# Performance work log

Hardware: AMD Instinct MI355X
Metric: run time of the kernel (lower is better)

## Reference

```python
import jax, jax.numpy as jnp
import numpy as np

H = 100  # hidden_size
D = 300  # input/output feature dim (hardcoded in module)
T = 32768  # number of timesteps


def _lstm_layer(x_seq, W_ih, W_hh, b_ih, b_hh):
    """Single LSTM layer over time. x_seq: [T, H_in]. PyTorch gate order i,f,g,o."""
    Hh = W_hh.shape[1]
    b = b_ih + b_hh
    # precompute input projection for all timesteps (removes per-step GEMM)
    x_proj = x_seq @ W_ih.T + b  # [T, 4H]

    def step(carry, xp_t):
        h, c = carry
        gates = xp_t + h @ W_hh.T  # [4H]
        i, f, g, o = jnp.split(gates, 4, axis=-1)
        c = jax.nn.sigmoid(f) * c + jax.nn.sigmoid(i) * jnp.tanh(g)
        h = jax.nn.sigmoid(o) * jnp.tanh(c)
        return (h, c), h

    h0 = jnp.zeros((Hh,), x_seq.dtype)
    c0 = jnp.zeros((Hh,), x_seq.dtype)
    (h_T, c_T), hs = jax.lax.scan(step, (h0, c0), x_proj)
    return hs, h_T, c_T


def setup_inputs() -> dict:
    key = jax.random.key(0)
    ks = jax.random.split(key, 14)
    s = 0.08
    return {
        "inputs": jax.random.normal(ks[0], (T, D), jnp.float32),
        "W_inp": jax.random.normal(ks[1], (H, D), jnp.float32) * s,
        "b_inp": jax.random.normal(ks[2], (H,), jnp.float32) * s,
        "W_ih_l0": jax.random.normal(ks[3], (4 * H, H), jnp.float32) * s,
        "W_hh_l0": jax.random.normal(ks[4], (4 * H, H), jnp.float32) * s,
        "b_ih_l0": jax.random.normal(ks[5], (4 * H,), jnp.float32) * s,
        "b_hh_l0": jax.random.normal(ks[6], (4 * H,), jnp.float32) * s,
        "W_ih_l1": jax.random.normal(ks[7], (4 * H, H), jnp.float32) * s,
        "W_hh_l1": jax.random.normal(ks[8], (4 * H, H), jnp.float32) * s,
        "b_ih_l1": jax.random.normal(ks[9], (4 * H,), jnp.float32) * s,
        "b_hh_l1": jax.random.normal(ks[10], (4 * H,), jnp.float32) * s,
        "W_out": jax.random.normal(ks[11], (D, H), jnp.float32) * s,
        "b_out": jax.random.normal(ks[12], (D,), jnp.float32) * s,
    }


def reference(inputs, W_inp, b_inp, W_ih_l0, W_hh_l0, b_ih_l0, b_hh_l0,
              W_ih_l1, W_hh_l1, b_ih_l1, b_hh_l1, W_out, b_out):
    # teacher-forced forward (force=True): input projection for all steps at once
    x = inputs @ W_inp.T + b_inp  # [T, H]
    h0_seq, h0_T, c0_T = _lstm_layer(x, W_ih_l0, W_hh_l0, b_ih_l0, b_hh_l0)
    h1_seq, h1_T, c1_T = _lstm_layer(h0_seq, W_ih_l1, W_hh_l1, b_ih_l1, b_hh_l1)
    outputs = h1_seq @ W_out.T + b_out  # [T, D]
    h_n = jnp.stack([h0_T, h1_T])  # [2, H] final hidden per layer
    c_n = jnp.stack([c0_T, c1_T])  # [2, H] final cell per layer
    return outputs, h_n, c_n
```

## Files before the change

### kernel.cpp

```cpp
#include <hip/hip_runtime.h>

#define T_STEPS 32768
#define OUT_BASE 9830400

typedef _Float16 h2 __attribute__((ext_vector_type(2)));

#define H2BC(f_) __builtin_bit_cast(h2, f_)

__device__ __forceinline__ float fdot2(h2 a, h2 b, float c) {
#if __has_builtin(__builtin_amdgcn_fdot2)
    return __builtin_amdgcn_fdot2(a, b, c, false);
#else
    return c + (float)a.x * (float)b.x + (float)a.y * (float)b.y;
#endif
}

__device__ __forceinline__ float sigf(float x) { return 1.f / (1.f + __expf(-x)); }

__device__ __forceinline__ float tanh_f(float x) {
    float a = fabsf(x);
    float e = __expf(-2.f * a);
    float t = (1.f - e) / (1.f + e);
    return x < 0.f ? -t : t;
}

template <int CTRL>
__device__ __forceinline__ float qperm(float x) {
#if __has_builtin(__builtin_amdgcn_update_dpp)
    return __builtin_bit_cast(
        float, __builtin_amdgcn_update_dpp(0, __builtin_bit_cast(int, x), CTRL, 0xF, 0xF, true));
#else
    return __shfl_xor(x, CTRL == 0xB1 ? 1 : (CTRL == 0x4E ? 2 : 3));
#endif
}

__device__ __forceinline__ void bar_lds() {
    asm volatile("s_waitcnt lgkmcnt(0)\n\ts_barrier" ::: "memory");
}

__global__ void k_precomp(const float* __restrict__ W_inp, const float* __restrict__ b_inp,
                          const float* __restrict__ W_ih0, const float* __restrict__ b_ih0,
                          const float* __restrict__ b_hh0,
                          float* __restrict__ Wc, float* __restrict__ bc) {
    int idx = blockIdx.x * 256 + threadIdx.x;
    if (idx < 120000) {
        int r = idx / 300, d = idx % 300;
        float acc = 0.f;
        for (int h = 0; h < 100; h++) acc += W_ih0[r * 100 + h] * W_inp[h * 300 + d];
        Wc[idx] = acc;
    } else if (idx < 120400) {
        int r = idx - 120000;
        float acc = b_ih0[r] + b_hh0[r];
        for (int h = 0; h < 100; h++) acc += W_ih0[r * 100 + h] * b_inp[h];
        bc[r] = acc;
    }
}

__global__ __launch_bounds__(512) void k_xproj(const float* __restrict__ inp,
                                               const float* __restrict__ Wc,
                                               const float* __restrict__ bc,
                                               _Float16* __restrict__ x0p) {
    __shared__ float xs[32 * 300];
    int t0 = blockIdx.x * 32;
    for (int idx = threadIdx.x; idx < 9600; idx += 512) xs[idx] = inp[(size_t)t0 * 300 + idx];
    __syncthreads();
    int j = threadIdx.x;
    if (j < 400) {
        float acc[32];
#pragma unroll
        for (int i = 0; i < 32; i++) acc[i] = 0.f;
        const float4* w4 = (const float4*)(Wc + j * 300);
        const float4* x4 = (const float4*)xs;
        for (int d4 = 0; d4 < 75; d4++) {
            float4 w = w4[d4];
#pragma unroll
            for (int ti = 0; ti < 32; ti++) {
                float4 x = x4[ti * 75 + d4];
                acc[ti] += w.x * x.x + w.y * x.y + w.z * x.z + w.w * x.w;
            }
        }
        float bb = bc[j];
        int dst = (j % 100) * 4 + j / 100;
#pragma unroll
        for (int ti = 0; ti < 32; ti++)
            x0p[(size_t)(t0 + ti) * 400 + dst] = (_Float16)(acc[ti] + bb);
    }
}


#define TICK0(T_, XREG_, TNEXT_, P_) do {                                                    \
    if (j < 400) {                                                                           \
        float xc_ = XREG_;                                                                   \
        int tn_ = (TNEXT_) < T_STEPS ? (TNEXT_) : T_STEPS - 1;                               \
        XREG_ = (float)x0p[(size_t)tn_ * 400 + j];                                           \
        const float4* h4_ = (const float4*)hbuf[P_];                                         \
        float aa_ = xc_, ab_ = 0.f, ac_ = 0.f, ad_ = 0.f;                                    \
        _Pragma("unroll")                                                                    \
        for (int c_ = 0; c_ < 12; c_++) {                                                    \
            float4 v_ = h4_[c_];                                                             \
            aa_ = fdot2(w0[4 * c_ + 0], H2BC(v_.x), aa_);                                    \
            ab_ = fdot2(w0[4 * c_ + 1], H2BC(v_.y), ab_);                                    \
            ac_ = fdot2(w0[4 * c_ + 2], H2BC(v_.z), ac_);                                    \
            ad_ = fdot2(w0[4 * c_ + 3], H2BC(v_.w), ad_);                                    \
        }                                                                                    \
        { float2 v_ = *(const float2*)((const char*)hbuf[P_] + 192);                         \
          aa_ = fdot2(w0[48], H2BC(v_.x), aa_);                                              \
          ab_ = fdot2(w0[49], H2BC(v_.y), ab_); }                                            \
        float s0_ = (aa_ + ab_) + (ac_ + ad_);                                               \
        float nl_ = __builtin_fmaf(sigf(s0_ * s_), s_, addc_);                               \
        float fg_ = qperm<0xB1>(nl_), gg_ = qperm<0x4E>(nl_), og_ = qperm<0x1B>(nl_);        \
        if ((j & 3) == 0) {                                                                  \
            int u_ = j >> 2;                                                                 \
            c0 = fg_ * c0 + nl_ * gg_;                                                       \
            float h0v_ = og_ * tanh_f(c0);                                                   \
            hbuf[1 - (P_)][u_] = (_Float16)h0v_;                                             \
            if ((T_) == T_STEPS - 1) { outTail[u_] = h0v_; outTail[200 + u_] = c0; }         \
        }                                                                                    \
    } else if (j >= 448) {                                                                   \
        int k_ = j - 448;                                                                    \
        if (k_ < 50 && (T_) >= 1) {                                                          \
            unsigned v_ = ((const unsigned*)hbuf[P_])[k_];                                   \
            __hip_atomic_store(&h0seq[(size_t)((T_) - 1) * 50 + k_], v_,                     \
                               __ATOMIC_RELAXED, __HIP_MEMORY_SCOPE_AGENT);                  \
        }                                                                                    \
        if (k_ == 0 && ((T_) & 7) == 7)                                                      \
            __hip_atomic_store(flag, (unsigned)(T_),                                         \
                               __ATOMIC_RELEASE, __HIP_MEMORY_SCOPE_AGENT);                  \
    }                                                                                        \
    bar_lds();                                                                               \
} while (0)

#define TICK1(T_, P_, WREG_, LREG_) do {                                                     \
    if (j < 400) {                                                                           \
        const char* hb_ = (const char*)hbuf[P_];                                             \
        const float4* u0_ = (const float4*)hb_;                                              \
        const float4* u1_ = (const float4*)(hb_ + 208);                                      \
        float aa_ = b1c, ab_ = 0.f, ac_ = 0.f, ad_ = 0.f;                                    \
        _Pragma("unroll")                                                                    \
        for (int c_ = 0; c_ < 12; c_++) {                                                    \
            float4 v_ = u0_[c_];                                                             \
            aa_ = fdot2(w1[4 * c_ + 0], H2BC(v_.x), aa_);                                    \
            ab_ = fdot2(w1[4 * c_ + 1], H2BC(v_.y), ab_);                                    \
            ac_ = fdot2(w1[4 * c_ + 2], H2BC(v_.z), ac_);                                    \
            ad_ = fdot2(w1[4 * c_ + 3], H2BC(v_.w), ad_);                                    \
        }                                                                                    \
        { float2 v_ = *(const float2*)(hb_ + 192);                                           \
          aa_ = fdot2(w1[48], H2BC(v_.x), aa_);                                              \
          ab_ = fdot2(w1[49], H2BC(v_.y), ab_); }                                            \
        _Pragma("unroll")                                                                    \
        for (int c_ = 0; c_ < 12; c_++) {                                                    \
            float4 v_ = u1_[c_];                                                             \
            aa_ = fdot2(w1[50 + 4 * c_ + 0], H2BC(v_.x), aa_);                               \
            ab_ = fdot2(w1[50 + 4 * c_ + 1], H2BC(v_.y), ab_);                               \
            ac_ = fdot2(w1[50 + 4 * c_ + 2], H2BC(v_.z), ac_);                               \
            ad_ = fdot2(w1[50 + 4 * c_ + 3], H2BC(v_.w), ad_);                               \
        }                                                                                    \
        { float2 v_ = *(const float2*)(hb_ + 400);                                           \
          aa_ = fdot2(w1[98], H2BC(v_.x), aa_);                                              \
          ab_ = fdot2(w1[99], H2BC(v_.y), ab_); }                                            \
        float s1_ = (aa_ + ab_) + (ac_ + ad_);                                               \
        float nl_ = __builtin_fmaf(sigf(s1_ * s_), s_, addc_);                               \
        float fg_ = qperm<0xB1>(nl_), gg_ = qperm<0x4E>(nl_), og_ = qperm<0x1B>(nl_);        \
        if ((j & 3) == 0) {                                                                  \
            int u_ = j >> 2;                                                                 \
            c1 = fg_ * c1 + nl_ * gg_;                                                       \
            float h1v_ = og_ * tanh_f(c1);                                                   \
            hbuf[1 - (P_)][104 + u_] = (_Float16)h1v_;                                       \
            h1s[(size_t)(T_) * 100 + u_] = h1v_;                                             \
            if ((T_) == T_STEPS - 1) { outTail[100 + u_] = h1v_; outTail[300 + u_] = c1; }   \
        }                                                                                    \
    } else if (j >= 448) {                                                                   \
        int k_ = j - 448;                                                                    \
        if (k_ < 50) {                                                                       \
            if ((T_) + 1 < T_STEPS) ((unsigned*)hbuf[1 - (P_)])[k_] = WREG_;                 \
            if ((T_) + 2 < T_STEPS) {                                                        \
                int need_ = (T_) + 3;                                                        \
                if ((int)fcache < need_) {                                                   \
                    unsigned f_;                                                             \
                    while ((int)(f_ = __hip_atomic_load(flag, __ATOMIC_RELAXED,              \
                                                        __HIP_MEMORY_SCOPE_AGENT)) < need_) \
                        __builtin_amdgcn_s_sleep(2);                                         \
                    fcache = f_;                                                             \
                    asm volatile("" ::: "memory");                                           \
                }                                                                            \
                LREG_ = __hip_atomic_load(&h0seq[(size_t)((T_) + 2) * 50 + k_],              \
                                          __ATOMIC_RELAXED, __HIP_MEMORY_SCOPE_AGENT);       \
            }                                                                                \
        }                                                                                    \
    }                                                                                        \
    bar_lds();                                                                               \
} while (0)

__global__ __launch_bounds__(512) __attribute__((amdgpu_waves_per_eu(2, 2)))
void k_scan2(const _Float16* __restrict__ x0p,
             const float* __restrict__ Whh0,
             const float* __restrict__ Wih1,
             const float* __restrict__ Whh1,
             const float* __restrict__ bih1,
             const float* __restrict__ bhh1,
             float* __restrict__ h1s,
             float* __restrict__ outTail,
             unsigned* __restrict__ h0seq,
             unsigned* __restrict__ flag) {
    __shared__ __align__(16) _Float16 hbuf[2][208];
    const int j = threadIdx.x;
    const int g4 = j & 3;
    const float s_ = (g4 == 2) ? 2.f : 1.f;
    const float addc_ = (g4 == 2) ? -1.f : 0.f;

    if (blockIdx.x == 0) {
        h2 w0[50];
        float xa = 0.f, xb = 0.f, c0 = 0.f;
        if (j < 400) {
            int r = g4 * 100 + (j >> 2);
            const float2* p0 = (const float2*)(Whh0 + r * 100);
#pragma unroll
            for (int k = 0; k < 50; k++) { float2 v = p0[k]; h2 q; q.x = (_Float16)v.x; q.y = (_Float16)v.y; w0[k] = q; }
            xa = (float)x0p[j];
            xb = (float)x0p[400 + j];
        }
        if (j < 208) ((unsigned*)hbuf)[j] = 0u;
        __syncthreads();

        for (int t = 0; t < T_STEPS; t += 2) {
            TICK0(t, xa, t + 2, 0);
            TICK0(t + 1, xb, t + 3, 1);
        }
        if (j >= 448) {
            int k = j - 448;
            if (k < 50) {
                unsigned v = ((const unsigned*)hbuf[0])[k];
                __hip_atomic_store(&h0seq[(size_t)(T_STEPS - 1) * 50 + k], v,
                                   __ATOMIC_RELAXED, __HIP_MEMORY_SCOPE_AGENT);
            }
            if (k == 0)
                __hip_atomic_store(flag, (unsigned)T_STEPS,
                                   __ATOMIC_RELEASE, __HIP_MEMORY_SCOPE_AGENT);
        }
    } else {
        h2 w1[100];
        float b1c = 0.f, c1 = 0.f;
        unsigned vA = 0, vB = 0, fcache = 0;
        if (j < 400) {
            int r = g4 * 100 + (j >> 2);
            const float2* p1 = (const float2*)(Wih1 + r * 100);
#pragma unroll
            for (int k = 0; k < 50; k++) { float2 v = p1[k]; h2 q; q.x = (_Float16)v.x; q.y = (_Float16)v.y; w1[k] = q; }
            const float2* p2 = (const float2*)(Whh1 + r * 100);
#pragma unroll
            for (int k = 0; k < 50; k++) { float2 v = p2[k]; h2 q; q.x = (_Float16)v.x; q.y = (_Float16)v.y; w1[50 + k] = q; }
            b1c = bih1[r] + bhh1[r];
        }
        if (j < 208) ((unsigned*)hbuf)[j] = 0u;
        __syncthreads();
        if (j >= 448) {
            int k = j - 448;
            unsigned f_;
            while ((int)(f_ = __hip_atomic_load(flag, __ATOMIC_RELAXED, __HIP_MEMORY_SCOPE_AGENT)) < 2)
                __builtin_amdgcn_s_sleep(8);
            fcache = f_;
            asm volatile("" ::: "memory");
            if (k < 50) {
                vA = __hip_atomic_load(&h0seq[k], __ATOMIC_RELAXED, __HIP_MEMORY_SCOPE_AGENT);
                vB = __hip_atomic_load(&h0seq[50 + k], __ATOMIC_RELAXED, __HIP_MEMORY_SCOPE_AGENT);
                ((unsigned*)hbuf[0])[k] = vA;
            }
        }
        __syncthreads();

        for (int t = 0; t < T_STEPS; t += 2) {
            TICK1(t, 0, vB, vA);
            TICK1(t + 1, 1, vA, vB);
        }
    }
}

__global__ __launch_bounds__(320) void k_out(const float* __restrict__ h1s,
                                             const float* __restrict__ Wout,
                                             const float* __restrict__ bout,
                                             float* __restrict__ out) {
    __shared__ float hs[32 * 100];
    int t0 = blockIdx.x * 32;
    for (int idx = threadIdx.x; idx < 3200; idx += 320) hs[idx] = h1s[(size_t)t0 * 100 + idx];
    __syncthreads();
    int d = threadIdx.x;
    if (d < 300) {
        float acc[32];
#pragma unroll
        for (int i = 0; i < 32; i++) acc[i] = 0.f;
        const float4* w4 = (const float4*)(Wout + d * 100);
        const float4* h4 = (const float4*)hs;
        for (int j4 = 0; j4 < 25; j4++) {
            float4 w = w4[j4];
#pragma unroll
            for (int ti = 0; ti < 32; ti++) {
                float4 h = h4[ti * 25 + j4];
                acc[ti] += w.x * h.x + w.y * h.y + w.z * h.z + w.w * h.w;
            }
        }
        float bb = bout[d];
#pragma unroll
        for (int ti = 0; ti < 32; ti++) out[(size_t)(t0 + ti) * 300 + d] = acc[ti] + bb;
    }
}

extern "C" void kernel_launch(void* const* d_in, const int* in_sizes, int n_in,
                              void* d_out, int out_size, void* d_ws, size_t ws_size,
                              hipStream_t stream) {
    const float* inputs = (const float*)d_in[0];
    const float* W_inp  = (const float*)d_in[1];
    const float* b_inp  = (const float*)d_in[2];
    const float* W_ih0  = (const float*)d_in[3];
    const float* W_hh0  = (const float*)d_in[4];
    const float* b_ih0  = (const float*)d_in[5];
    const float* b_hh0  = (const float*)d_in[6];
    const float* W_ih1  = (const float*)d_in[7];
    const float* W_hh1  = (const float*)d_in[8];
    const float* b_ih1  = (const float*)d_in[9];
    const float* b_hh1  = (const float*)d_in[10];
    const float* W_out  = (const float*)d_in[11];
    const float* b_out  = (const float*)d_in[12];
    float* out = (float*)d_out;

    char* ws = (char*)d_ws;
    _Float16* x0p = (_Float16*)ws;
    float* h1s = (float*)(ws + 26214400);
    float* Wc  = (float*)(ws + 26214400 + 13107200);
    float* bc  = Wc + 120000;

    unsigned* h0seq = (unsigned*)out;
    unsigned* flagp = (unsigned*)out + 1638400;
    float* outTail = out + OUT_BASE;

    hipMemsetAsync(flagp, 0, 4, stream);
    k_precomp<<<471, 256, 0, stream>>>(W_inp, b_inp, W_ih0, b_ih0, b_hh0, Wc, bc);
    k_xproj<<<1024, 512, 0, stream>>>(inputs, Wc, bc, x0p);

    void* args[] = {(void*)&x0p, (void*)&W_hh0, (void*)&W_ih1, (void*)&W_hh1,
                    (void*)&b_ih1, (void*)&b_hh1, (void*)&h1s, (void*)&outTail,
                    (void*)&h0seq, (void*)&flagp};
    hipLaunchCooperativeKernel((void*)k_scan2, dim3(2), dim3(512), args, 0, stream);

    k_out<<<1024, 320, 0, stream>>>(h1s, W_out, b_out, out);
}
```

Baseline: 25.42 ms.

## Split each gate-row dot product across lane pairs to halve per-thread serial work

Each thread now computes half of two gate rows' dot products (one K-half for gate pair A and B), and the halves are combined via a DPP lane swap. The LDS hidden buffer is padded so each half reads its own 112-byte region. This shortens the per-step serial FMA chain on the recurrence critical path in both LSTM layers. In exchange it adds extra cross-lane permutes and a select, and it changes the hidden-vector layout and the h0seq copy indexing.

```diff
diff --git a/kernel.cpp b/kernel.cpp
--- a/kernel.cpp
+++ b/kernel.cpp
@@ -4,8 +4,12 @@
 #define OUT_BASE 9830400
 
 typedef _Float16 h2 __attribute__((ext_vector_type(2)));
-
 #define H2BC(f_) __builtin_bit_cast(h2, f_)
+
+#define ALD(p)     __hip_atomic_load((p), __ATOMIC_RELAXED, __HIP_MEMORY_SCOPE_AGENT)
+#define AST(p, v)  __hip_atomic_store((p), (v), __ATOMIC_RELAXED, __HIP_MEMORY_SCOPE_AGENT)
+#define ASTR(p, v) __hip_atomic_store((p), (v), __ATOMIC_RELEASE, __HIP_MEMORY_SCOPE_AGENT)
+#define CFENCE()   asm volatile("" ::: "memory")
 
 __device__ __forceinline__ float fdot2(h2 a, h2 b, float c) {
 #if __has_builtin(__builtin_amdgcn_fdot2)
@@ -36,6 +40,30 @@
 
 __device__ __forceinline__ void bar_lds() {
     asm volatile("s_waitcnt lgkmcnt(0)\n\ts_barrier" ::: "memory");
+}
+
+__device__ __forceinline__ void ldw(h2* w, const float* p) {
+#pragma unroll
+    for (int k = 0; k < 25; k++) {
+        float2 v = ((const float2*)p)[k];
+        h2 t; t.x = (_Float16)v.x; t.y = (_Float16)v.y; w[k] = t;
+    }
+}
+
+__device__ __forceinline__ float2 mv25(const h2* wA, const h2* wB, const char* rec) {
+    const float4* hv = (const float4*)rec;
+    float pA = 0.f, pB = 0.f;
+#pragma unroll
+    for (int c = 0; c < 6; c++) {
+        float4 v = hv[c];
+        pA = fdot2(wA[4 * c + 0], H2BC(v.x), pA); pB = fdot2(wB[4 * c + 0], H2BC(v.x), pB);
+        pA = fdot2(wA[4 * c + 1], H2BC(v.y), pA); pB = fdot2(wB[4 * c + 1], H2BC(v.y), pB);
+        pA = fdot2(wA[4 * c + 2], H2BC(v.z), pA); pB = fdot2(wB[4 * c + 2], H2BC(v.z), pB);
+        pA = fdot2(wA[4 * c + 3], H2BC(v.w), pA); pB = fdot2(wB[4 * c + 3], H2BC(v.w), pB);
+    }
+    float vl = *(const float*)(rec + 96);
+    pA = fdot2(wA[24], H2BC(vl), pA); pB = fdot2(wB[24], H2BC(vl), pB);
+    return make_float2(pA, pB);
 }
 
 __global__ void k_precomp(const float* __restrict__ W_inp, const float* __restrict__ b_inp,
@@ -88,103 +116,60 @@
 }
 
 
-#define TICK0(T_, XREG_, TNEXT_, P_) do {                                                    \
+#define B0TICK(T_, XR_, P_) do {                                                             \
     if (j < 400) {                                                                           \
-        float xc_ = XREG_;                                                                   \
-        int tn_ = (TNEXT_) < T_STEPS ? (TNEXT_) : T_STEPS - 1;                               \
-        XREG_ = (float)x0p[(size_t)tn_ * 400 + j];                                           \
-        const float4* h4_ = (const float4*)hbuf[P_];                                         \
-        float aa_ = xc_, ab_ = 0.f, ac_ = 0.f, ad_ = 0.f;                                    \
-        _Pragma("unroll")                                                                    \
-        for (int c_ = 0; c_ < 12; c_++) {                                                    \
-            float4 v_ = h4_[c_];                                                             \
-            aa_ = fdot2(w0[4 * c_ + 0], H2BC(v_.x), aa_);                                    \
-            ab_ = fdot2(w0[4 * c_ + 1], H2BC(v_.y), ab_);                                    \
-            ac_ = fdot2(w0[4 * c_ + 2], H2BC(v_.z), ac_);                                    \
-            ad_ = fdot2(w0[4 * c_ + 3], H2BC(v_.w), ad_);                                    \
-        }                                                                                    \
-        { float2 v_ = *(const float2*)((const char*)hbuf[P_] + 192);                         \
-          aa_ = fdot2(w0[48], H2BC(v_.x), aa_);                                              \
-          ab_ = fdot2(w0[49], H2BC(v_.y), ab_); }                                            \
-        float s0_ = (aa_ + ab_) + (ac_ + ad_);                                               \
-        float nl_ = __builtin_fmaf(sigf(s0_ * s_), s_, addc_);                               \
+        float xc_ = XR_;                                                                     \
+        int tn_ = (T_) + 2 < T_STEPS ? (T_) + 2 : T_STEPS - 1;                               \
+        XR_ = (float)x0p[(size_t)tn_ * 400 + j];                                             \
+        float2 p_ = mv25(wA, wB, (const char*)lds[P_] + hoff);                               \
+        float pA_ = p_.x + qperm<0xB1>(p_.x);                                                \
+        float pB_ = p_.y + qperm<0xB1>(p_.y);                                                \
+        float sv_ = (H ? pB_ : pA_) + xc_;                                                   \
+        float nl_ = __builtin_fmaf(sigf(sv_ * s_), s_, addc_);                               \
         float fg_ = qperm<0xB1>(nl_), gg_ = qperm<0x4E>(nl_), og_ = qperm<0x1B>(nl_);        \
-        if ((j & 3) == 0) {                                                                  \
-            int u_ = j >> 2;                                                                 \
+        if (q == 0) {                                                                        \
             c0 = fg_ * c0 + nl_ * gg_;                                                       \
             float h0v_ = og_ * tanh_f(c0);                                                   \
-            hbuf[1 - (P_)][u_] = (_Float16)h0v_;                                             \
-            if ((T_) == T_STEPS - 1) { outTail[u_] = h0v_; outTail[200 + u_] = c0; }         \
+            ((_Float16*)lds[1 - (P_)])[hidx] = (_Float16)h0v_;                               \
+            if ((T_) == T_STEPS - 1) { outTail[u] = h0v_; outTail[200 + u] = c0; }           \
         }                                                                                    \
     } else if (j >= 448) {                                                                   \
-        int k_ = j - 448;                                                                    \
-        if (k_ < 50 && (T_) >= 1) {                                                          \
-            unsigned v_ = ((const unsigned*)hbuf[P_])[k_];                                   \
-            __hip_atomic_store(&h0seq[(size_t)((T_) - 1) * 50 + k_], v_,                     \
-                               __ATOMIC_RELAXED, __HIP_MEMORY_SCOPE_AGENT);                  \
-        }                                                                                    \
-        if (k_ == 0 && ((T_) & 7) == 7)                                                      \
-            __hip_atomic_store(flag, (unsigned)(T_),                                         \
-                               __ATOMIC_RELEASE, __HIP_MEMORY_SCOPE_AGENT);                  \
+        if (kk < 50 && (T_) >= 1)                                                            \
+            AST(&h0seq[(size_t)((T_) - 1) * 50 + kk], lds[P_][pidx]);                        \
+        if (kk == 0 && (((T_) & 7) == 7)) ASTR(&flags[0], (unsigned)(T_));                   \
     }                                                                                        \
     bar_lds();                                                                               \
 } while (0)
 
-#define TICK1(T_, P_, WREG_, LREG_) do {                                                     \
+#define B1TICK(T_, P_, WREG_, LREG_) do {                                                    \
     if (j < 400) {                                                                           \
-        const char* hb_ = (const char*)hbuf[P_];                                             \
-        const float4* u0_ = (const float4*)hb_;                                              \
-        const float4* u1_ = (const float4*)(hb_ + 208);                                      \
-        float aa_ = b1c, ab_ = 0.f, ac_ = 0.f, ad_ = 0.f;                                    \
-        _Pragma("unroll")                                                                    \
-        for (int c_ = 0; c_ < 12; c_++) {                                                    \
-            float4 v_ = u0_[c_];                                                             \
-            aa_ = fdot2(w1[4 * c_ + 0], H2BC(v_.x), aa_);                                    \
-            ab_ = fdot2(w1[4 * c_ + 1], H2BC(v_.y), ab_);                                    \
-            ac_ = fdot2(w1[4 * c_ + 2], H2BC(v_.z), ac_);                                    \
-            ad_ = fdot2(w1[4 * c_ + 3], H2BC(v_.w), ad_);                                    \
-        }                                                                                    \
-        { float2 v_ = *(const float2*)(hb_ + 192);                                           \
-          aa_ = fdot2(w1[48], H2BC(v_.x), aa_);                                              \
-          ab_ = fdot2(w1[49], H2BC(v_.y), ab_); }                                            \
-        _Pragma("unroll")                                                                    \
-        for (int c_ = 0; c_ < 12; c_++) {                                                    \
-            float4 v_ = u1_[c_];                                                             \
-            aa_ = fdot2(w1[50 + 4 * c_ + 0], H2BC(v_.x), aa_);                               \
-            ab_ = fdot2(w1[50 + 4 * c_ + 1], H2BC(v_.y), ab_);                               \
-            ac_ = fdot2(w1[50 + 4 * c_ + 2], H2BC(v_.z), ac_);                               \
-            ad_ = fdot2(w1[50 + 4 * c_ + 3], H2BC(v_.w), ad_);                               \
-        }                                                                                    \
-        { float2 v_ = *(const float2*)(hb_ + 400);                                           \
-          aa_ = fdot2(w1[98], H2BC(v_.x), aa_);                                              \
-          ab_ = fdot2(w1[99], H2BC(v_.y), ab_); }                                            \
-        float s1_ = (aa_ + ab_) + (ac_ + ad_);                                               \
-        float nl_ = __builtin_fmaf(sigf(s1_ * s_), s_, addc_);                               \
+        const char* hb_ = (const char*)lds[P_];                                              \
+        float2 p0_ = mv25(wA0, wB0, hb_ + hoff);                          \
+        float2 p1_ = mv25(wA1, wB1, hb_ + 224 + hoff);                  \
+        float pA_ = p0_.x + p1_.x;  pA_ += qperm<0xB1>(pA_);                                 \
+        float pB_ = p0_.y + p1_.y;  pB_ += qperm<0xB1>(pB_);                                 \
+        float sv_ = (H ? pB_ : pA_) + bz;                                                    \
+        float nl_ = __builtin_fmaf(sigf(sv_ * s_), s_, addc_);                               \
         float fg_ = qperm<0xB1>(nl_), gg_ = qperm<0x4E>(nl_), og_ = qperm<0x1B>(nl_);        \
-        if ((j & 3) == 0) {                                                                  \
-            int u_ = j >> 2;                                                                 \
+        if (q == 0) {                                                                        \
             c1 = fg_ * c1 + nl_ * gg_;                                                       \
             float h1v_ = og_ * tanh_f(c1);                                                   \
-            hbuf[1 - (P_)][104 + u_] = (_Float16)h1v_;                                       \
-            h1s[(size_t)(T_) * 100 + u_] = h1v_;                                             \
-            if ((T_) == T_STEPS - 1) { outTail[100 + u_] = h1v_; outTail[300 + u_] = c1; }   \
+            ((_Float16*)(lds[1 - (P_)] + 56))[hidx] = (_Float16)h1v_;                        \
+            h1s[(size_t)(T_) * 100 + u] = h1v_;                                              \
+            if ((T_) == T_STEPS - 1) { outTail[100 + u] = h1v_; outTail[300 + u] = c1; }     \
         }                                                                                    \
     } else if (j >= 448) {                                                                   \
-        int k_ = j - 448;                                                                    \
-        if (k_ < 50) {                                                                       \
-            if ((T_) + 1 < T_STEPS) ((unsigned*)hbuf[1 - (P_)])[k_] = WREG_;                 \
+        if (kk < 50) {                                                                       \
+            if ((T_) + 1 < T_STEPS) lds[1 - (P_)][pidx] = WREG_;                             \
             if ((T_) + 2 < T_STEPS) {                                                        \
-                int need_ = (T_) + 3;                                                        \
-                if ((int)fcache < need_) {                                                   \
+                unsigned need_ = (unsigned)(T_) + 3u;                                        \
+                if (fcache < need_) {                                                        \
                     unsigned f_;                                                             \
-                    while ((int)(f_ = __hip_atomic_load(flag, __ATOMIC_RELAXED,              \
-                                                        __HIP_MEMORY_SCOPE_AGENT)) < need_) \
-                        __builtin_amdgcn_s_sleep(2);                                         \
+                    while ((f_ = ALD(flags)) < need_) __builtin_amdgcn_s_sleep(2);           \
                     fcache = f_;                                                             \
-                    asm volatile("" ::: "memory");                                           \
+                    CFENCE();                                                                \
                 }                                                                            \
-                LREG_ = __hip_atomic_load(&h0seq[(size_t)((T_) + 2) * 50 + k_],              \
-                                          __ATOMIC_RELAXED, __HIP_MEMORY_SCOPE_AGENT);       \
+                LREG_ = ALD(&h0seq[(size_t)((T_) + 2) * 50 + kk]);                           \
             }                                                                                \
         }                                                                                    \
     }                                                                                        \
@@ -201,76 +186,69 @@
              float* __restrict__ h1s,
              float* __restrict__ outTail,
              unsigned* __restrict__ h0seq,
-             unsigned* __restrict__ flag) {
-    __shared__ __align__(16) _Float16 hbuf[2][208];
+             unsigned* __restrict__ flags) {
+    __shared__ __align__(16) unsigned lds[2][112];
     const int j = threadIdx.x;
-    const int g4 = j & 3;
-    const float s_ = (g4 == 2) ? 2.f : 1.f;
-    const float addc_ = (g4 == 2) ? -1.f : 0.f;
+    const int q = j & 3, u = j >> 2, H = q & 1, gA = (q >> 1) * 2;
+    const int hoff = H * 112;
+    const int hidx = (u < 50) ? u : 56 + (u - 50);
+    const int kk = j - 448;
+    const int pidx = (kk < 25) ? kk : kk + 3;
+    const float s_ = (q == 2) ? 2.f : 1.f;
+    const float addc_ = (q == 2) ? -1.f : 0.f;
 
     if (blockIdx.x == 0) {
-        h2 w0[50];
+        h2 wA[25], wB[25];
         float xa = 0.f, xb = 0.f, c0 = 0.f;
         if (j < 400) {
-            int r = g4 * 100 + (j >> 2);
-            const float2* p0 = (const float2*)(Whh0 + r * 100);
-#pragma unroll
-            for (int k = 0; k < 50; k++) { float2 v = p0[k]; h2 q; q.x = (_Float16)v.x; q.y = (_Float16)v.y; w0[k] = q; }
+            int r0 = gA * 100 + u;
+            ldw(wA, Whh0 + r0 * 100 + 50 * H);
+            ldw(wB, Whh0 + (r0 + 100) * 100 + 50 * H);
             xa = (float)x0p[j];
             xb = (float)x0p[400 + j];
         }
-        if (j < 208) ((unsigned*)hbuf)[j] = 0u;
+        if (j < 224) ((unsigned*)lds)[j] = 0u;
         __syncthreads();
 
         for (int t = 0; t < T_STEPS; t += 2) {
-            TICK0(t, xa, t + 2, 0);
-            TICK0(t + 1, xb, t + 3, 1);
+            B0TICK(t, xa, 0);
+            B0TICK(t + 1, xb, 1);
         }
         if (j >= 448) {
-            int k = j - 448;
-            if (k < 50) {
-                unsigned v = ((const unsigned*)hbuf[0])[k];
-                __hip_atomic_store(&h0seq[(size_t)(T_STEPS - 1) * 50 + k], v,
-                                   __ATOMIC_RELAXED, __HIP_MEMORY_SCOPE_AGENT);
-            }
-            if (k == 0)
-                __hip_atomic_store(flag, (unsigned)T_STEPS,
-                                   __ATOMIC_RELEASE, __HIP_MEMORY_SCOPE_AGENT);
+            if (kk < 50) AST(&h0seq[(size_t)(T_STEPS - 1) * 50 + kk], lds[0][pidx]);
+            if (kk == 0) ASTR(&flags[0], (unsigned)T_STEPS);
         }
     } else {
-        h2 w1[100];
-        float b1c = 0.f, c1 = 0.f;
+        h2 wA0[25], wB0[25], wA1[25], wB1[25];
+        float bz = 0.f, c1 = 0.f;
         unsigned vA = 0, vB = 0, fcache = 0;
         if (j < 400) {
-            int r = g4 * 100 + (j >> 2);
-            const float2* p1 = (const float2*)(Wih1 + r * 100);
-#pragma unroll
-            for (int k = 0; k < 50; k++) { float2 v = p1[k]; h2 q; q.x = (_Float16)v.x; q.y = (_Float16)v.y; w1[k] = q; }
-            const float2* p2 = (const float2*)(Whh1 + r * 100);
-#pragma unroll
-            for (int k = 0; k < 50; k++) { float2 v = p2[k]; h2 q; q.x = (_Float16)v.x; q.y = (_Float16)v.y; w1[50 + k] = q; }
-            b1c = bih1[r] + bhh1[r];
-        }
-        if (j < 208) ((unsigned*)hbuf)[j] = 0u;
+            int r0 = gA * 100 + u;
+            ldw(wA0, Wih1 + r0 * 100 + 50 * H);
+            ldw(wB0, Wih1 + (r0 + 100) * 100 + 50 * H);
+            ldw(wA1, Whh1 + r0 * 100 + 50 * H);
+            ldw(wB1, Whh1 + (r0 + 100) * 100 + 50 * H);
+            int ro = q * 100 + u;
+            bz = bih1[ro] + bhh1[ro];
+        }
+        if (j < 224) ((unsigned*)lds)[j] = 0u;
         __syncthreads();
         if (j >= 448) {
-            int k = j - 448;
             unsigned f_;
-            while ((int)(f_ = __hip_atomic_load(flag, __ATOMIC_RELAXED, __HIP_MEMORY_SCOPE_AGENT)) < 2)
-                __builtin_amdgcn_s_sleep(8);
+            while ((f_ = ALD(flags)) < 2u) __builtin_amdgcn_s_sleep(8);
             fcache = f_;
-            asm volatile("" ::: "memory");
-            if (k < 50) {
-                vA = __hip_atomic_load(&h0seq[k], __ATOMIC_RELAXED, __HIP_MEMORY_SCOPE_AGENT);
-                vB = __hip_atomic_load(&h0seq[50 + k], __ATOMIC_RELAXED, __HIP_MEMORY_SCOPE_AGENT);
-                ((unsigned*)hbuf[0])[k] = vA;
+            CFENCE();
+            if (kk < 50) {
+                vA = ALD(&h0seq[kk]);
+                vB = ALD(&h0seq[50 + kk]);
+                lds[0][pidx] = vA;
             }
         }
         __syncthreads();
 
         for (int t = 0; t < T_STEPS; t += 2) {
-            TICK1(t, 0, vB, vA);
-            TICK1(t + 1, 1, vA, vB);
+            B1TICK(t, 0, vB, vA);
+            B1TICK(t + 1, 1, vA, vB);
         }
     }
 }
```

Measured after the change: 23.91 ms. -6.0%, faster.
